# Kernel tuning notes

Hardware: AMD Instinct MI355X
Metric: run time of the kernel (lower is better)

## Reference

```python
import jax, jax.numpy as jnp
import numpy as np

BLANK = 59  # CFG['pad_phrase'] == blank_index == label pad value
NEG = jnp.float32(-1e30)  # -inf surrogate safe for logaddexp


def setup_inputs() -> dict:
    key = jax.random.key(0)
    k1, k2 = jax.random.split(key)
    B, T, V, L = 1024, 384, 60, 45
    labels = jax.random.randint(k1, (B, L), 0, BLANK, dtype=jnp.int32)
    logits = jax.random.normal(k2, (B, T, V), dtype=jnp.float32)
    return {"labels": labels, "logits": logits}


def _ctc_loss(logits, labels):
    # logits: [B, T, V] (not time-major), labels: [B, L] padded with BLANK
    B, T, V = logits.shape
    L = labels.shape[1]
    S = 2 * L + 1  # extended label length: blanks interleaved

    logp = jax.nn.log_softmax(logits, axis=-1)  # tf.nn.ctc_loss softmaxes internally

    # extended label sequence: [blank, l1, blank, l2, ..., blank]
    ext = jnp.full((B, S), BLANK, dtype=jnp.int32).at[:, 1::2].set(labels)
    # per-step emission log-probs for each extended-label position: [B, T, S]
    emit = jnp.take_along_axis(logp, ext[:, None, :], axis=2)

    # skip transition s-2 -> s allowed iff s >= 2, ext[s] != blank, ext[s] != ext[s-2]
    ext_m2 = jnp.pad(ext[:, :-2], ((0, 0), (2, 0)), constant_values=-1)
    skip_ok = (jnp.arange(S) >= 2) & (ext != BLANK) & (ext != ext_m2)

    # alpha init at t=0: only positions 0 (blank) and 1 (first label) reachable
    alpha0 = jnp.full((B, S), NEG).at[:, 0].set(emit[:, 0, 0]).at[:, 1].set(emit[:, 0, 1])

    def step(alpha, emit_t):
        s1 = jnp.pad(alpha[:, :-1], ((0, 0), (1, 0)), constant_values=NEG)
        s2 = jnp.where(skip_ok, jnp.pad(alpha[:, :-2], ((0, 0), (2, 0)), constant_values=NEG), NEG)
        alpha = jnp.logaddexp(jnp.logaddexp(alpha, s1), s2) + emit_t
        return alpha, None

    emit_tbs = jnp.swapaxes(emit, 0, 1)  # [T, B, S]
    alpha_T, _ = jax.lax.scan(step, alpha0, emit_tbs[1:])

    # label_length = number of non-pad tokens (as in the TF layer)
    label_len = jnp.sum((labels != BLANK).astype(jnp.int32), axis=-1)
    end = 2 * label_len  # index of final blank in extended sequence
    a_blank = jnp.take_along_axis(alpha_T, end[:, None], axis=1)[:, 0]
    a_label = jnp.take_along_axis(alpha_T, jnp.maximum(end - 1, 0)[:, None], axis=1)[:, 0]
    a_label = jnp.where(end > 0, a_label, NEG)
    nll = -jnp.logaddexp(a_blank, a_label)  # [B]
    return jnp.mean(nll)


def reference(labels, logits):
    return _ctc_loss(logits, labels)
```

## Files before the change

### kernel.cpp

```cpp
#include <hip/hip_runtime.h>
#include <hip/hip_fp16.h>

#define BLANKC 59

typedef _Float16 half8 __attribute__((ext_vector_type(8)));
typedef _Float16 half4 __attribute__((ext_vector_type(4)));

#define LDS_FENCE() asm volatile("s_waitcnt lgkmcnt(0)" ::: "memory")

__device__ __forceinline__ float wave_shr1(float x, float fill) {
    int r = __builtin_amdgcn_update_dpp(__float_as_int(fill), __float_as_int(x),
                                        0x138 , 0xF, 0xF, false);
    return __int_as_float(r);
}
__device__ __forceinline__ float wave_shl1(float x, float fill) {
    int r = __builtin_amdgcn_update_dpp(__float_as_int(fill), __float_as_int(x),
                                        0x130 , 0xF, 0xF, false);
    return __int_as_float(r);
}

template <int CTRL>
__device__ __forceinline__ float dpp_fmax(float x) {
    int r = __builtin_amdgcn_update_dpp(__float_as_int(x), __float_as_int(x),
                                        CTRL, 0xF, 0xF, false);
    return fmaxf(x, __int_as_float(r));
}
template <int CTRL>
__device__ __forceinline__ float dpp_addf(float x) {
    int r = __builtin_amdgcn_update_dpp(__float_as_int(x), __float_as_int(x),
                                        CTRL, 0xF, 0xF, false);
    return x + __int_as_float(r);
}
__device__ __forceinline__ float wave_max_bcast(float x) {
    x = dpp_fmax<0x111>(x); x = dpp_fmax<0x112>(x);
    x = dpp_fmax<0x114>(x); x = dpp_fmax<0x118>(x);
    x = dpp_fmax<0x142>(x); x = dpp_fmax<0x143>(x);
    return __int_as_float(__builtin_amdgcn_readlane(__float_as_int(x), 63));
}
__device__ __forceinline__ float wave_sum_bcast(float x) {
    x = dpp_addf<0x111>(x); x = dpp_addf<0x112>(x);
    x = dpp_addf<0x114>(x); x = dpp_addf<0x118>(x);
    x = dpp_addf<0x142>(x); x = dpp_addf<0x143>(x);
    return __int_as_float(__builtin_amdgcn_readlane(__float_as_int(x), 63));
}

#define SCRS 68
#define SDS  24

__global__ __launch_bounds__(128)
void ctc_fused(const int* __restrict__ labels, const float* __restrict__ logits,
               float* __restrict__ out, int T, int V, int L, float inv_b) {
    const int b    = blockIdx.x;
    const int tid  = threadIdx.x;
    const int lane = tid & 63;
    const int wid  = tid >> 6;

    __shared__ __align__(16) __half scr[2][8][SCRS];
    __shared__ __align__(16) __half Sd[2][46 * SDS];
    __shared__ float fa0[64], fa1[64];
    __shared__ int   labs[2][64];
    __shared__ int   esF_s, wdone;

    labs[wid][lane] = (lane < L) ? labels[(long)b * L + lane] : BLANKC;
    if (tid == 0) wdone = 0;
    __syncthreads();

    const int* mylab = labs[wid];

    const int tq = lane >> 3;
    const int q  = lane & 7;
    const int c0 = q * 8;
    const bool full = (q < 7);
    const float* src = logits + (long)b * T * V;

    int gl[6], gr[6], gv[6]; bool gok[6];
    #pragma unroll
    for (int k = 0; k < 6; ++k) {
        const int i = lane + (k << 6);
        gok[k] = (i < 368);
        gl[k] = i >> 3; gr[k] = i & 7;
        gv[k] = (gok[k] && gl[k] < 45) ? mylab[gl[k]] : BLANKC;
    }

    const int labL = (lane < L) ? mylab[lane] : BLANKC;
    const int labP = (lane >= 1 && lane < L) ? mylab[lane - 1] : BLANKC;
    const float skipf = ((lane >= 1) && (lane < L) && (labL != BLANKC) && (labL != labP))
                        ? 1.0f : 0.0f;
    const unsigned long long mk = __ballot((lane < L) && (labL != BLANKC));
    const int len = __popcll(mk);

    const int rl = (lane < 45) ? lane : 45;
    const __half* rowL = &Sd[wid][rl * SDS];
    const __half* rowB = &Sd[wid][45 * SDS];
    const half8 hz = {};

    auto ld = [&](int ch, float4& P0, float4& P1) {
        const float* p = src + (ch * 8 + tq) * 60 + c0;
        P0 = *(const float4*)p;
        if (full) P1 = *(const float4*)(p + 4);
    };
    auto smx_gather = [&](float e0, float e1, float e2, float e3,
                          float e4, float e5, float e6, float e7) {
        float s = ((e0 + e1) + (e2 + e3)) + ((e4 + e5) + (e6 + e7));
        s = dpp_addf<0xB1>(s);
        s = dpp_addf<0x4E>(s);
        s += __shfl_xor(s, 4, 64);
        const float inv = __builtin_amdgcn_rcpf(s);
        const half4 p0 = { (_Float16)(e0 * inv), (_Float16)(e1 * inv),
                           (_Float16)(e2 * inv), (_Float16)(e3 * inv) };
        const half4 p1 = { (_Float16)(e4 * inv), (_Float16)(e5 * inv),
                           (_Float16)(e6 * inv), (_Float16)(e7 * inv) };
        *(half4*)&scr[wid][tq][c0]     = p0;
        *(half4*)&scr[wid][tq][c0 + 4] = p1;
        LDS_FENCE();
        #pragma unroll
        for (int k = 0; k < 6; ++k)
            if (gok[k]) Sd[wid][gl[k] * SDS + gr[k]] = scr[wid][gr[k]][gv[k]];
        LDS_FENCE();
    };

    if (wid == 0) {
        float a0 = 0.f, a1 = 0.f;
        int esum = 80;
        auto step = [&](float eL, float eB) {
            const float p   = wave_shr1(a1, 0.0f);
            const float t1  = a0 + a1;
            const float na0 = (a0 + p) * eB;
            const float na1 = fmaf(skipf, p, t1) * eL;
            a0 = na0; a1 = na1;
        };
        auto renorm = [&]() {
            const float m = wave_max_bcast(fmaxf(a0, a1));
            const int e = (__float_as_int(m) >> 23) & 0xff;
            int sexp = 207 - e;
            if (sexp > 127) sexp = 127;
            const float sc = __int_as_float((sexp + 127) << 23);
            a0 *= sc; a1 *= sc;
            esum += sexp;
        };
        auto body = [&](int ch, int pre, float4& P0, float4& P1, bool first) {
            const float e0 = __expf(P0.x), e1 = __expf(P0.y),
                        e2 = __expf(P0.z), e3 = __expf(P0.w);
            float e4 = 0.f, e5 = 0.f, e6 = 0.f, e7 = 0.f;
            if (full) { e4 = __expf(P1.x); e5 = __expf(P1.y);
                        e6 = __expf(P1.z); e7 = __expf(P1.w); }
            if (pre >= 0) ld(pre, P0, P1);
            smx_gather(e0, e1, e2, e3, e4, e5, e6, e7);
            half8 cL = *(const half8*)rowL;
            half8 cB = *(const half8*)rowB;
            if (lane >= 45) cL = hz;
            if (lane >= 46) cB = hz;
            if (first) {
                a0 = (lane == 0) ? (float)cB[0] * 0x1p80f : 0.f;
                a1 = (lane == 0) ? (float)cL[0] * 0x1p80f : 0.f;
                #pragma unroll
                for (int i = 1; i < 8; ++i) step((float)cL[i], (float)cB[i]);
            } else {
                #pragma unroll
                for (int i = 0; i < 8; ++i) step((float)cL[i], (float)cB[i]);
            }
            renorm();
        };
        float4 X0, X1{0.f,0.f,0.f,0.f}, Y0, Y1{0.f,0.f,0.f,0.f};
        ld(0, X0, X1); ld(1, Y0, Y1);
        for (int c = 0; c < 24; c += 2) {
            body(c,     (c + 2 < 24) ? c + 2 : -1, X0, X1, c == 0);
            body(c + 1, (c + 3 < 24) ? c + 3 : -1, Y0, Y1, false);
        }
        fa0[lane] = a0;
        fa1[lane] = a1;
        if (lane == 0) esF_s = esum;
        LDS_FENCE();
        if (lane == 0)
            __hip_atomic_store(&wdone, 1, __ATOMIC_RELAXED,
                               __HIP_MEMORY_SCOPE_WORKGROUP);
        return;
    }

    float g0 = (lane == len) ? 0x1p80f : 0.f;
    float g1 = (lane == len - 1) ? 0x1p80f : 0.f;
    int esum = 80;
    auto bstep = [&](float eL, float eB) {
        const float h0 = g0 * eB;
        const float h1 = g1 * eL;
        const float qq = wave_shl1(fmaf(skipf, h1, h0), 0.0f);
        g0 = h0 + h1;
        g1 = h1 + qq;
    };
    auto renormB = [&]() {
        const float m = wave_max_bcast(fmaxf(g0, g1));
        const int e = (__float_as_int(m) >> 23) & 0xff;
        int sexp = 207 - e;
        if (sexp > 127) sexp = 127;
        const float sc = __int_as_float((sexp + 127) << 23);
        g0 *= sc; g1 *= sc;
        esum += sexp;
    };
    auto bodyb = [&](int ch, int pre, float4& P0, float4& P1) {
        const float e0 = __expf(P0.x), e1 = __expf(P0.y),
                    e2 = __expf(P0.z), e3 = __expf(P0.w);
        float e4 = 0.f, e5 = 0.f, e6 = 0.f, e7 = 0.f;
        if (full) { e4 = __expf(P1.x); e5 = __expf(P1.y);
                    e6 = __expf(P1.z); e7 = __expf(P1.w); }
        if (pre >= 0) ld(pre, P0, P1);
        smx_gather(e0, e1, e2, e3, e4, e5, e6, e7);
        half8 cL = *(const half8*)rowL;
        half8 cB = *(const half8*)rowB;
        if (lane >= 45) cL = hz;
        if (lane >= 46) cB = hz;
        #pragma unroll
        for (int i = 7; i >= 0; --i) bstep((float)cL[i], (float)cB[i]);
        renormB();
    };
    float4 X0, X1{0.f,0.f,0.f,0.f}, Y0, Y1{0.f,0.f,0.f,0.f};
    ld(47, X0, X1); ld(46, Y0, Y1);
    for (int k = 0; k < 24; k += 2) {
        bodyb(47 - k,       (k + 2 < 24) ? 47 - (k + 2) : -1, X0, X1);
        bodyb(47 - (k + 1), (k + 3 < 24) ? 47 - (k + 3) : -1, Y0, Y1);
    }

    int d = __hip_atomic_load(&wdone, __ATOMIC_RELAXED, __HIP_MEMORY_SCOPE_WORKGROUP);
    while (!d) {
        __builtin_amdgcn_s_sleep(1);
        d = __hip_atomic_load(&wdone, __ATOMIC_RELAXED, __HIP_MEMORY_SCOPE_WORKGROUP);
    }
    asm volatile("" ::: "memory");
    const float t0 = __log2f(fa0[lane]) + __log2f(g0);
    const float t1 = __log2f(fa1[lane]) + __log2f(g1);
    const float m  = wave_max_bcast(fmaxf(t0, t1));
    const float tt = wave_sum_bcast(exp2f(t0 - m) + exp2f(t1 - m));
    if (lane == 0) {
        const float log2P = m + __log2f(tt) - (float)(esum + esF_s);
        const float nll = -0.69314718055994531f * log2P;
        atomicAdd(out, nll * inv_b);
    }
}

extern "C" void kernel_launch(void* const* d_in, const int* in_sizes, int n_in,
                              void* d_out, int out_size, void* d_ws, size_t ws_size,
                              hipStream_t stream) {
    const int* labels   = (const int*)d_in[0];
    const float* logits = (const float*)d_in[1];
    float* out          = (float*)d_out;
    (void)d_ws; (void)ws_size;

    const int L = 45, V = 60;
    const int B = in_sizes[0] / L;
    const int T = in_sizes[1] / (B * V);

    hipMemsetAsync(out, 0, (size_t)out_size * sizeof(float), stream);
    ctc_fused<<<B, 128, 0, stream>>>(labels, logits, out, T, V, L, 1.0f / (float)B);
}
```

Before: 155.3 us.

## Replace fp16 two-stage LDS gather with fp32 transposed softmax scratch and deeper prefetch

Removes the half-precision scratch and the separate gather pass into the Sd buffer. Each lane now writes fp32 probabilities transposed by vocabulary index, then reads its own label row and the blank row directly as float4 pairs. That cuts one LDS fence and the 6-way scattered gather per chunk. Global prefetch depth grows from 2 to 6 chunks per wave, and the t=0 initialisation is folded into a uniform scaled start state with lane masks. The risks are higher register pressure from 12 buffered float4s and possible LDS bank conflicts from the stride-12 transposed writes.

```diff
diff --git a/kernel.cpp b/kernel.cpp
--- a/kernel.cpp
+++ b/kernel.cpp
@@ -2,9 +2,6 @@
 #include <hip/hip_fp16.h>
 
 #define BLANKC 59
-
-typedef _Float16 half8 __attribute__((ext_vector_type(8)));
-typedef _Float16 half4 __attribute__((ext_vector_type(4)));
 
 #define LDS_FENCE() asm volatile("s_waitcnt lgkmcnt(0)" ::: "memory")
 
@@ -43,9 +40,6 @@
     x = dpp_addf<0x142>(x); x = dpp_addf<0x143>(x);
     return __int_as_float(__builtin_amdgcn_readlane(__float_as_int(x), 63));
 }
-
-#define SCRS 68
-#define SDS  24
 
 __global__ __launch_bounds__(128)
 void ctc_fused(const int* __restrict__ labels, const float* __restrict__ logits,
@@ -55,8 +49,7 @@
     const int lane = tid & 63;
     const int wid  = tid >> 6;
 
-    __shared__ __align__(16) __half scr[2][8][SCRS];
-    __shared__ __align__(16) __half Sd[2][46 * SDS];
+    __shared__ float scrF[2][64 * 12];
     __shared__ float fa0[64], fa1[64];
     __shared__ int   labs[2][64];
     __shared__ int   esF_s, wdone;
@@ -66,21 +59,11 @@
     __syncthreads();
 
     const int* mylab = labs[wid];
-
     const int tq = lane >> 3;
     const int q  = lane & 7;
     const int c0 = q * 8;
     const bool full = (q < 7);
     const float* src = logits + (long)b * T * V;
-
-    int gl[6], gr[6], gv[6]; bool gok[6];
-    #pragma unroll
-    for (int k = 0; k < 6; ++k) {
-        const int i = lane + (k << 6);
-        gok[k] = (i < 368);
-        gl[k] = i >> 3; gr[k] = i & 7;
-        gv[k] = (gok[k] && gl[k] < 45) ? mylab[gl[k]] : BLANKC;
-    }
 
     const int labL = (lane < L) ? mylab[lane] : BLANKC;
     const int labP = (lane >= 1 && lane < L) ? mylab[lane - 1] : BLANKC;
@@ -88,45 +71,56 @@
                         ? 1.0f : 0.0f;
     const unsigned long long mk = __ballot((lane < L) && (labL != BLANKC));
     const int len = __popcll(mk);
-
-    const int rl = (lane < 45) ? lane : 45;
-    const __half* rowL = &Sd[wid][rl * SDS];
-    const __half* rowB = &Sd[wid][45 * SDS];
-    const half8 hz = {};
+    const float mL = (lane <= 44) ? 1.f : 0.f;
+    const float mB = (lane <= 45) ? 1.f : 0.f;
+
+    const int labv = (lane < 45) ? mylab[lane] : BLANKC;
+    const int prow = ((labv & 7) << 3) | (labv >> 3);
+    float* scw = &scrF[wid][0];
+    const float* rL = &scrF[wid][prow * 12];
+    const float* rB = &scrF[wid][31 * 12];
 
     auto ld = [&](int ch, float4& P0, float4& P1) {
         const float* p = src + (ch * 8 + tq) * 60 + c0;
         P0 = *(const float4*)p;
         if (full) P1 = *(const float4*)(p + 4);
     };
-    auto smx_gather = [&](float e0, float e1, float e2, float e3,
-                          float e4, float e5, float e6, float e7) {
+
+    auto produce = [&](float4& P0, float4& P1, int prech,
+                       float4& l0, float4& l1, float4& b0, float4& b1) {
+        const float e0 = __expf(P0.x), e1 = __expf(P0.y),
+                    e2 = __expf(P0.z), e3 = __expf(P0.w);
+        float e4 = 0.f, e5 = 0.f, e6 = 0.f, e7 = 0.f;
+        if (full) { e4 = __expf(P1.x); e5 = __expf(P1.y);
+                    e6 = __expf(P1.z); e7 = __expf(P1.w); }
+        if (prech >= 0) ld(prech, P0, P1);
         float s = ((e0 + e1) + (e2 + e3)) + ((e4 + e5) + (e6 + e7));
         s = dpp_addf<0xB1>(s);
         s = dpp_addf<0x4E>(s);
         s += __shfl_xor(s, 4, 64);
         const float inv = __builtin_amdgcn_rcpf(s);
-        const half4 p0 = { (_Float16)(e0 * inv), (_Float16)(e1 * inv),
-                           (_Float16)(e2 * inv), (_Float16)(e3 * inv) };
-        const half4 p1 = { (_Float16)(e4 * inv), (_Float16)(e5 * inv),
-                           (_Float16)(e6 * inv), (_Float16)(e7 * inv) };
-        *(half4*)&scr[wid][tq][c0]     = p0;
-        *(half4*)&scr[wid][tq][c0 + 4] = p1;
+        scw[( 0 + q) * 12 + tq] = e0 * inv;
+        scw[( 8 + q) * 12 + tq] = e1 * inv;
+        scw[(16 + q) * 12 + tq] = e2 * inv;
+        scw[(24 + q) * 12 + tq] = e3 * inv;
+        scw[(32 + q) * 12 + tq] = e4 * inv;
+        scw[(40 + q) * 12 + tq] = e5 * inv;
+        scw[(48 + q) * 12 + tq] = e6 * inv;
+        scw[(56 + q) * 12 + tq] = e7 * inv;
         LDS_FENCE();
-        #pragma unroll
-        for (int k = 0; k < 6; ++k)
-            if (gok[k]) Sd[wid][gl[k] * SDS + gr[k]] = scr[wid][gr[k]][gv[k]];
-        LDS_FENCE();
+        l0 = *(const float4*)rL; l1 = *(const float4*)(rL + 4);
+        b0 = *(const float4*)rB; b1 = *(const float4*)(rB + 4);
     };
 
     if (wid == 0) {
-        float a0 = 0.f, a1 = 0.f;
+        float a0 = (lane == 0) ? 0x1p80f : 0.f;
+        float a1 = 0.f;
         int esum = 80;
         auto step = [&](float eL, float eB) {
             const float p   = wave_shr1(a1, 0.0f);
             const float t1  = a0 + a1;
-            const float na0 = (a0 + p) * eB;
-            const float na1 = fmaf(skipf, p, t1) * eL;
+            const float na0 = (a0 + p) * (eB * mB);
+            const float na1 = fmaf(skipf, p, t1) * (eL * mL);
             a0 = na0; a1 = na1;
         };
         auto renorm = [&]() {
@@ -138,34 +132,19 @@
             a0 *= sc; a1 *= sc;
             esum += sexp;
         };
-        auto body = [&](int ch, int pre, float4& P0, float4& P1, bool first) {
-            const float e0 = __expf(P0.x), e1 = __expf(P0.y),
-                        e2 = __expf(P0.z), e3 = __expf(P0.w);
-            float e4 = 0.f, e5 = 0.f, e6 = 0.f, e7 = 0.f;
-            if (full) { e4 = __expf(P1.x); e5 = __expf(P1.y);
-                        e6 = __expf(P1.z); e7 = __expf(P1.w); }
-            if (pre >= 0) ld(pre, P0, P1);
-            smx_gather(e0, e1, e2, e3, e4, e5, e6, e7);
-            half8 cL = *(const half8*)rowL;
-            half8 cB = *(const half8*)rowB;
-            if (lane >= 45) cL = hz;
-            if (lane >= 46) cB = hz;
-            if (first) {
-                a0 = (lane == 0) ? (float)cB[0] * 0x1p80f : 0.f;
-                a1 = (lane == 0) ? (float)cL[0] * 0x1p80f : 0.f;
-                #pragma unroll
-                for (int i = 1; i < 8; ++i) step((float)cL[i], (float)cB[i]);
-            } else {
-                #pragma unroll
-                for (int i = 0; i < 8; ++i) step((float)cL[i], (float)cB[i]);
+        float4 X0[6], X1[6];
+        #pragma unroll
+        for (int s = 0; s < 6; ++s) ld(s, X0[s], X1[s]);
+        for (int g = 0; g < 24; g += 6) {
+            #pragma unroll
+            for (int s = 0; s < 6; ++s) {
+                const int c = g + s;
+                float4 l0, l1, b0, b1;
+                produce(X0[s], X1[s], (c + 6 < 24) ? c + 6 : -1, l0, l1, b0, b1);
+                step(l0.x, b0.x); step(l0.y, b0.y); step(l0.z, b0.z); step(l0.w, b0.w);
+                step(l1.x, b1.x); step(l1.y, b1.y); step(l1.z, b1.z); step(l1.w, b1.w);
+                renorm();
             }
-            renorm();
-        };
-        float4 X0, X1{0.f,0.f,0.f,0.f}, Y0, Y1{0.f,0.f,0.f,0.f};
-        ld(0, X0, X1); ld(1, Y0, Y1);
-        for (int c = 0; c < 24; c += 2) {
-            body(c,     (c + 2 < 24) ? c + 2 : -1, X0, X1, c == 0);
-            body(c + 1, (c + 3 < 24) ? c + 3 : -1, Y0, Y1, false);
         }
         fa0[lane] = a0;
         fa1[lane] = a1;
@@ -181,8 +160,8 @@
     float g1 = (lane == len - 1) ? 0x1p80f : 0.f;
     int esum = 80;
     auto bstep = [&](float eL, float eB) {
-        const float h0 = g0 * eB;
-        const float h1 = g1 * eL;
+        const float h0 = g0 * (eB * mB);
+        const float h1 = g1 * (eL * mL);
         const float qq = wave_shl1(fmaf(skipf, h1, h0), 0.0f);
         g0 = h0 + h1;
         g1 = h1 + qq;
@@ -196,27 +175,21 @@
         g0 *= sc; g1 *= sc;
         esum += sexp;
     };
-    auto bodyb = [&](int ch, int pre, float4& P0, float4& P1) {
-        const float e0 = __expf(P0.x), e1 = __expf(P0.y),
-                    e2 = __expf(P0.z), e3 = __expf(P0.w);
-        float e4 = 0.f, e5 = 0.f, e6 = 0.f, e7 = 0.f;
-        if (full) { e4 = __expf(P1.x); e5 = __expf(P1.y);
-                    e6 = __expf(P1.z); e7 = __expf(P1.w); }
-        if (pre >= 0) ld(pre, P0, P1);
-        smx_gather(e0, e1, e2, e3, e4, e5, e6, e7);
-        half8 cL = *(const half8*)rowL;
-        half8 cB = *(const half8*)rowB;
-        if (lane >= 45) cL = hz;
-        if (lane >= 46) cB = hz;
+    {
+        float4 X0[6], X1[6];
         #pragma unroll
-        for (int i = 7; i >= 0; --i) bstep((float)cL[i], (float)cB[i]);
-        renormB();
-    };
-    float4 X0, X1{0.f,0.f,0.f,0.f}, Y0, Y1{0.f,0.f,0.f,0.f};
-    ld(47, X0, X1); ld(46, Y0, Y1);
-    for (int k = 0; k < 24; k += 2) {
-        bodyb(47 - k,       (k + 2 < 24) ? 47 - (k + 2) : -1, X0, X1);
-        bodyb(47 - (k + 1), (k + 3 < 24) ? 47 - (k + 3) : -1, Y0, Y1);
+        for (int s = 0; s < 6; ++s) ld(47 - s, X0[s], X1[s]);
+        for (int g = 0; g < 24; g += 6) {
+            #pragma unroll
+            for (int s = 0; s < 6; ++s) {
+                const int i = g + s;
+                float4 l0, l1, b0, b1;
+                produce(X0[s], X1[s], (i + 6 < 24) ? 47 - (i + 6) : -1, l0, l1, b0, b1);
+                bstep(l1.w, b1.w); bstep(l1.z, b1.z); bstep(l1.y, b1.y); bstep(l1.x, b1.x);
+                bstep(l0.w, b0.w); bstep(l0.z, b0.z); bstep(l0.y, b0.y); bstep(l0.x, b0.x);
+                renormB();
+            }
+        }
     }
 
     int d = __hip_atomic_load(&wdone, __ATOMIC_RELAXED, __HIP_MEMORY_SCOPE_WORKGROUP);
```

Result: no change. 153.4 us (-1.2%).
